# Kernel tuning notes

Measured on AMD Instinct MI355X. Metric: run time of the kernel, lower is better.

Reference implementation:

```python
import jax, jax.numpy as jnp
import numpy as np

MAX_SEQ_LEN = 2048
ADJ_SCALE = 0.1


def setup_inputs() -> dict:
    key = jax.random.key(0)
    k1, k2, k3 = jax.random.split(key, 3)
    B, L, H, D = 8, 2048, 16, 64
    x = jax.random.normal(k1, (B, L, H, D), dtype=jnp.float32)
    W = jax.random.normal(k2, (D, D), dtype=jnp.float32) * (1.0 / np.sqrt(D))
    b = jax.random.normal(k3, (D,), dtype=jnp.float32) * 0.02
    gate = jnp.ones((1,), dtype=jnp.float32) * 0.5  # betweenness_gate init
    return {"x": x, "W": W, "b": b, "gate": gate}


def reference(x, W, b, gate):
    B, L, H, D = x.shape
    # --- RoPE frequency table (precompute_freqs_cis) ---
    base_freqs = 1.0 / (10000.0 ** (jnp.arange(0, D, 2, dtype=jnp.float32) / D))  # (D/2,)
    t = jnp.arange(L, dtype=jnp.float32)
    freqs = t[:, None] * base_freqs[None, :]          # (L, D/2)
    fcos, fsin = jnp.cos(freqs), jnp.sin(freqs)

    # --- betweenness: only consecutive-pair distances are ever used ---
    content = jnp.einsum('blhd,ed->blhe', x, W) + b    # nn.Linear(dim, dim)
    d1 = jnp.linalg.norm(content[:, 1:] - content[:, :-1], axis=-1)   # (B, L-1, H)  d(i, i+1)
    d2 = jnp.linalg.norm(content[:, 2:] - content[:, :-2], axis=-1)   # (B, L-2, H)  d(i, i+2)
    direct = d2
    path = d1[:, :-1] + d1[:, 1:]
    score = jax.nn.relu(1.0 - (path - direct) / jnp.maximum(direct, 1e-6))  # (B, L-2, H)
    betweenness = jnp.zeros((B, L, H), x.dtype).at[:, 1:L - 1].set(score / (L - 2))

    # --- betweenness-adjusted interpolated RoPE (vectorized over positions) ---
    adjust = gate[0] * (betweenness - 0.5) * ADJ_SCALE               # (B, L, H)
    pos = jnp.arange(L, dtype=jnp.float32)[None, :, None]
    adj_pos = jnp.clip(pos + adjust, 0.0, MAX_SEQ_LEN - 1)
    lo = jnp.floor(adj_pos).astype(jnp.int32)
    hi = jnp.ceil(adj_pos).astype(jnp.int32)
    frac = (adj_pos - lo)[..., None]                                 # (B, L, H, 1)
    cos_i = (1.0 - frac) * fcos[lo] + frac * fcos[hi]                # (B, L, H, D/2)
    sin_i = (1.0 - frac) * fsin[lo] + frac * fsin[hi]

    x_even = x[..., 0::2]
    x_odd = x[..., 1::2]
    out_even = x_even * cos_i - x_odd * sin_i
    out_odd = x_odd * cos_i + x_even * sin_i
    out = jnp.stack([out_even, out_odd], axis=-1).reshape(B, L, H, D)  # re-interleave
    return out
```

## Files before the change

kernel.cpp:

```cpp
#include <hip/hip_runtime.h>

#define L_SEQ 2048
#define HEADS 16
#define DIM   64
#define TILE  32
#define XROWS 34
#define XPITCH 68
#define DROWS 48

typedef __attribute__((ext_vector_type(8))) short bf16x8;
typedef __attribute__((ext_vector_type(4))) float f32x4;

static __device__ __forceinline__ unsigned short f2bf_rtne(float f) {
    unsigned int u = __builtin_bit_cast(unsigned int, f);
    u += 0x7fffu + ((u >> 16) & 1u);
    return (unsigned short)(u >> 16);
}
static __device__ __forceinline__ unsigned int pk2(float a, float b) {
    return __builtin_amdgcn_perm(__builtin_bit_cast(unsigned int, b),
                                 __builtin_bit_cast(unsigned int, a), 0x07060302u);
}

#define SWZ(row, col) ((row) * 64 + ((col) ^ (((row) & 7) * 8)))

__global__ void prep_w_kernel(const float* __restrict__ W, unsigned short* __restrict__ wbf) {
    int i = blockIdx.x * 256 + threadIdx.x;
    if (i < DIM * DIM) wbf[i] = f2bf_rtne(W[i]);
}

static __device__ __forceinline__ bf16x8 load_bfrag(const unsigned short* wbf,
                                                    const float* W, int n, int k0) {
    if (wbf) return *(const bf16x8*)(wbf + n * 64 + k0);
    const float* wr = W + n * 64 + k0;
    float4 w0 = *(const float4*)wr;
    float4 w1 = *(const float4*)(wr + 4);
    uint4 p;
    p.x = pk2(w0.x, w0.y); p.y = pk2(w0.z, w0.w);
    p.z = pk2(w1.x, w1.y); p.w = pk2(w1.z, w1.w);
    return __builtin_bit_cast(bf16x8, p);
}

__global__ __launch_bounds__(256) void betweenness_rope_kernel(
    const float* __restrict__ x, const float* __restrict__ W,
    const unsigned short* __restrict__ wbf, const float* __restrict__ gate,
    float* __restrict__ out)
{
    __shared__ float xs[XROWS * XPITCH];
    __shared__ unsigned short dl[DROWS * 64];
    __shared__ float psq[4][36];
    __shared__ float ppr[4][36];
    __shared__ float2 fl[TILE];

    const int tid  = threadIdx.x;
    const int lane = tid & 63;
    const int wv   = tid >> 6;
    const int la   = lane & 15, lg = lane >> 4;
    const int l0   = blockIdx.x * TILE;
    const int h    = blockIdx.y;
    const int b    = blockIdx.z;
    const int bh_off = (b * L_SEQ * HEADS + h) * DIM;

    for (int c = tid; c < XROWS * 16; c += 256) {
        int r = c >> 4, q = c & 15;
        int g = max(0, min(L_SEQ - 1, l0 - 1 + r));
        *(float4*)&xs[r * XPITCH + q * 4] =
            *(const float4*)(x + bh_off + g * (HEADS * DIM) + q * 4);
    }
    __syncthreads();

    for (int r = tid >> 3; r < DROWS; r += 32) {
        int c0 = (tid & 7) * 8;
        uint4 o = {0u, 0u, 0u, 0u};
        if (r <= 32) {
            float4 a0 = *(float4*)&xs[r * XPITCH + c0];
            float4 a1 = *(float4*)&xs[r * XPITCH + c0 + 4];
            float4 b0 = *(float4*)&xs[(r + 1) * XPITCH + c0];
            float4 b1 = *(float4*)&xs[(r + 1) * XPITCH + c0 + 4];
            o.x = pk2(b0.x - a0.x, b0.y - a0.y);
            o.y = pk2(b0.z - a0.z, b0.w - a0.w);
            o.z = pk2(b1.x - a1.x, b1.y - a1.y);
            o.w = pk2(b1.z - a1.z, b1.w - a1.w);
        }
        *(uint4*)&dl[SWZ(r, c0)] = o;
    }
    __syncthreads();

    {
        bf16x8 b0 = load_bfrag(wbf, W, 16 * wv + la, lg * 8);
        bf16x8 b1 = load_bfrag(wbf, W, 16 * wv + la, lg * 8 + 32);
        f32x4 e0 = {0.f,0.f,0.f,0.f}, e1 = {0.f,0.f,0.f,0.f}, e2 = {0.f,0.f,0.f,0.f};
        {
            bf16x8 aA0 = *(const bf16x8*)&dl[SWZ(la,      lg * 8)];
            bf16x8 aA1 = *(const bf16x8*)&dl[SWZ(la,      lg * 8 + 32)];
            bf16x8 aB0 = *(const bf16x8*)&dl[SWZ(16 + la, lg * 8)];
            bf16x8 aB1 = *(const bf16x8*)&dl[SWZ(16 + la, lg * 8 + 32)];
            bf16x8 aC0 = *(const bf16x8*)&dl[SWZ(32 + la, lg * 8)];
            bf16x8 aC1 = *(const bf16x8*)&dl[SWZ(32 + la, lg * 8 + 32)];
            e0 = __builtin_amdgcn_mfma_f32_16x16x32_bf16(aA0, b0, e0, 0, 0, 0);
            e0 = __builtin_amdgcn_mfma_f32_16x16x32_bf16(aA1, b1, e0, 0, 0, 0);
            e1 = __builtin_amdgcn_mfma_f32_16x16x32_bf16(aB0, b0, e1, 0, 0, 0);
            e1 = __builtin_amdgcn_mfma_f32_16x16x32_bf16(aB1, b1, e1, 0, 0, 0);
            e2 = __builtin_amdgcn_mfma_f32_16x16x32_bf16(aC0, b0, e2, 0, 0, 0);
            e2 = __builtin_amdgcn_mfma_f32_16x16x32_bf16(aC1, b1, e2, 0, 0, 0);
        }
        float upA = __shfl(e0[0], (lane + 16) & 63);
        float upB = __shfl(e1[0], (lane + 16) & 63);
        float upC = __shfl(e2[0], (lane + 16) & 63);
        float sq0[4], sq1[4], pr0[4], pr1[4], sq2;
        #pragma unroll
        for (int q = 0; q < 4; ++q) { sq0[q] = e0[q] * e0[q]; sq1[q] = e1[q] * e1[q]; }
        sq2 = e2[0] * e2[0];
        #pragma unroll
        for (int q = 0; q < 3; ++q) { pr0[q] = e0[q] * e0[q + 1]; pr1[q] = e1[q] * e1[q + 1]; }
        pr0[3] = e0[3] * ((lg == 3) ? upB : upA);
        pr1[3] = e1[3] * ((lg == 3) ? upC : upB);
        #pragma unroll
        for (int m = 1; m < 16; m <<= 1) {
            #pragma unroll
            for (int q = 0; q < 4; ++q) {
                sq0[q] += __shfl_xor(sq0[q], m, 64);
                sq1[q] += __shfl_xor(sq1[q], m, 64);
                pr0[q] += __shfl_xor(pr0[q], m, 64);
                pr1[q] += __shfl_xor(pr1[q], m, 64);
            }
            sq2 += __shfl_xor(sq2, m, 64);
        }
        if (la == 0) {
            #pragma unroll
            for (int q = 0; q < 4; ++q) {
                psq[wv][4 * lg + q] = sq0[q];
                ppr[wv][4 * lg + q] = pr0[q];
            }
        } else if (la == 1) {
            #pragma unroll
            for (int q = 0; q < 4; ++q) {
                psq[wv][16 + 4 * lg + q] = sq1[q];
                ppr[wv][16 + 4 * lg + q] = pr1[q];
            }
        } else if (la == 2 && lg == 0) {
            psq[wv][32] = sq2;
        }
    }
    __syncthreads();

    if (tid < TILE) {
        const float gate0 = gate[0];
        int r = tid, l = l0 + r;
        float n1a = psq[0][r]     + psq[1][r]     + psq[2][r]     + psq[3][r];
        float n1b = psq[0][r + 1] + psq[1][r + 1] + psq[2][r + 1] + psq[3][r + 1];
        float gg  = ppr[0][r]     + ppr[1][r]     + ppr[2][r]     + ppr[3][r];
        float d1a = sqrtf(n1a), d1b = sqrtf(n1b);
        float dd  = sqrtf(fmaxf(n1a + n1b + 2.f * gg, 0.f));
        float sc  = fmaxf(1.f - ((d1a + d1b) - dd) / fmaxf(dd, 1e-6f), 0.f);
        float bet = (l >= 1 && l <= L_SEQ - 2) ? sc * (1.f / (L_SEQ - 2)) : 0.f;
        float adjust = gate0 * (bet - 0.5f) * 0.1f;
        float ap  = fminf(fmaxf((float)l + adjust, 0.f), (float)(L_SEQ - 1));
        float flo = floorf(ap);
        fl[r] = make_float2(flo, ap - flo);
    }
    __syncthreads();

    {
        const int j = lane & 31, half = lane >> 5;
        const float fjr = __builtin_exp2f(-0.4152410118609203f * (float)j)
                        * 0.15915494309189535f;
        const float cf = __builtin_amdgcn_cosf(fjr);
        const float sf = __builtin_amdgcn_sinf(fjr);
        const float cfm1 = cf - 1.0f;
        const int r0w = wv * 2 + half;
        const float* xbase = &xs[(r0w + 1) * XPITCH + 2 * j];
        float* obase = out + bh_off + (l0 + r0w) * (HEADS * DIM) + 2 * j;
        #pragma unroll
        for (int it = 0; it < 4; ++it) {
            int r = it * 8 + r0w;
            float2 ff = fl[r];
            float t0 = ff.x * fjr;
            float rv = t0 - floorf(t0);
            float c_lo = __builtin_amdgcn_cosf(rv);
            float s_lo = __builtin_amdgcn_sinf(rv);
            float u = fmaf(ff.y, cfm1, 1.0f);
            float v = ff.y * sf;
            float ci = fmaf(-s_lo, v, c_lo * u);
            float si = fmaf(c_lo, v, s_lo * u);
            float2 xv = *(const float2*)(xbase + it * 8 * XPITCH);
            float2 o;
            o.x = xv.x * ci - xv.y * si;
            o.y = fmaf(xv.y, ci, xv.x * si);
            *(float2*)(obase + it * 8 * (HEADS * DIM)) = o;
        }
    }
}

extern "C" void kernel_launch(void* const* d_in, const int* in_sizes, int n_in,
                              void* d_out, int out_size, void* d_ws, size_t ws_size,
                              hipStream_t stream) {
    const float* x    = (const float*)d_in[0];
    const float* W    = (const float*)d_in[1];
    const float* gate = (const float*)d_in[3];
    float* out = (float*)d_out;

    const int B = in_sizes[0] / (L_SEQ * HEADS * DIM);

    unsigned short* wbf = nullptr;
    if (ws_size >= (size_t)(DIM * DIM * sizeof(unsigned short))) {
        wbf = (unsigned short*)d_ws;
        prep_w_kernel<<<16, 256, 0, stream>>>(W, wbf);
    }

    dim3 grid(L_SEQ / TILE, HEADS, B);
    betweenness_rope_kernel<<<grid, 256, 0, stream>>>(x, W, wbf, gate, out);
}
```

Before: 50.15 us.

## Use Gram matrix W^T W for consecutive-diff norms and fuse diff into load

Precomputes M = W^T W in a small prep kernel and stores it in bf16 in a device global. The main kernel then computes each squared norm and adjacent inner product as d^T M d and d_{i+1}^T M d_i via MFMA plus a short dot product. This replaces the old per-row output reductions, which needed many cross-lane shuffles. The bf16 row differences are now built straight from global loads while filling the x tile, which removes one shared-memory pass and one barrier. In exchange, each x row is read twice from global memory, and bf16 rounding of M adds some error.

```diff
diff --git a/kernel.cpp b/kernel.cpp
--- a/kernel.cpp
+++ b/kernel.cpp
@@ -11,6 +11,8 @@
 typedef __attribute__((ext_vector_type(8))) short bf16x8;
 typedef __attribute__((ext_vector_type(4))) float f32x4;
 
+__device__ unsigned short g_mbf[DIM * DIM];
+
 static __device__ __forceinline__ unsigned short f2bf_rtne(float f) {
     unsigned int u = __builtin_bit_cast(unsigned int, f);
     u += 0x7fffu + ((u >> 16) & 1u);
@@ -20,35 +22,32 @@
     return __builtin_amdgcn_perm(__builtin_bit_cast(unsigned int, b),
                                  __builtin_bit_cast(unsigned int, a), 0x07060302u);
 }
+static __device__ __forceinline__ float bfhi(unsigned int u) {
+    return __builtin_bit_cast(float, u << 16);
+}
+static __device__ __forceinline__ float bflo(unsigned int u) {
+    return __builtin_bit_cast(float, u & 0xffff0000u);
+}
 
 #define SWZ(row, col) ((row) * 64 + ((col) ^ (((row) & 7) * 8)))
 
-__global__ void prep_w_kernel(const float* __restrict__ W, unsigned short* __restrict__ wbf) {
-    int i = blockIdx.x * 256 + threadIdx.x;
-    if (i < DIM * DIM) wbf[i] = f2bf_rtne(W[i]);
-}
-
-static __device__ __forceinline__ bf16x8 load_bfrag(const unsigned short* wbf,
-                                                    const float* W, int n, int k0) {
-    if (wbf) return *(const bf16x8*)(wbf + n * 64 + k0);
-    const float* wr = W + n * 64 + k0;
-    float4 w0 = *(const float4*)wr;
-    float4 w1 = *(const float4*)(wr + 4);
-    uint4 p;
-    p.x = pk2(w0.x, w0.y); p.y = pk2(w0.z, w0.w);
-    p.z = pk2(w1.x, w1.y); p.w = pk2(w1.z, w1.w);
-    return __builtin_bit_cast(bf16x8, p);
+__global__ void prep_m_kernel(const float* __restrict__ W) {
+    const int i = blockIdx.x, j = threadIdx.x;
+    float acc = 0.f;
+    #pragma unroll 8
+    for (int e = 0; e < DIM; ++e)
+        acc = fmaf(W[e * DIM + i], W[e * DIM + j], acc);
+    g_mbf[i * DIM + j] = f2bf_rtne(acc);
 }
 
 __global__ __launch_bounds__(256) void betweenness_rope_kernel(
-    const float* __restrict__ x, const float* __restrict__ W,
-    const unsigned short* __restrict__ wbf, const float* __restrict__ gate,
+    const float* __restrict__ x, const float* __restrict__ gate,
     float* __restrict__ out)
 {
     __shared__ float xs[XROWS * XPITCH];
     __shared__ unsigned short dl[DROWS * 64];
-    __shared__ float psq[4][36];
-    __shared__ float ppr[4][36];
+    __shared__ float psq[4][DROWS];
+    __shared__ float ppr[4][DROWS];
     __shared__ float2 fl[TILE];
 
     const int tid  = threadIdx.x;
@@ -60,85 +59,65 @@
     const int b    = blockIdx.z;
     const int bh_off = (b * L_SEQ * HEADS + h) * DIM;
 
-    for (int c = tid; c < XROWS * 16; c += 256) {
-        int r = c >> 4, q = c & 15;
-        int g = max(0, min(L_SEQ - 1, l0 - 1 + r));
-        *(float4*)&xs[r * XPITCH + q * 4] =
-            *(const float4*)(x + bh_off + g * (HEADS * DIM) + q * 4);
-    }
-    __syncthreads();
-
-    for (int r = tid >> 3; r < DROWS; r += 32) {
-        int c0 = (tid & 7) * 8;
-        uint4 o = {0u, 0u, 0u, 0u};
-        if (r <= 32) {
-            float4 a0 = *(float4*)&xs[r * XPITCH + c0];
-            float4 a1 = *(float4*)&xs[r * XPITCH + c0 + 4];
-            float4 b0 = *(float4*)&xs[(r + 1) * XPITCH + c0];
-            float4 b1 = *(float4*)&xs[(r + 1) * XPITCH + c0 + 4];
-            o.x = pk2(b0.x - a0.x, b0.y - a0.y);
-            o.y = pk2(b0.z - a0.z, b0.w - a0.w);
-            o.z = pk2(b1.x - a1.x, b1.y - a1.y);
-            o.w = pk2(b1.z - a1.z, b1.w - a1.w);
+    for (int s = tid; s < 392; s += 256) {
+        if (s < 272) {
+            int r = s >> 3, c0 = (s & 7) * 8;
+            int g = max(0, min(L_SEQ - 1, l0 - 1 + r));
+            const float* px = x + bh_off + g * (HEADS * DIM) + c0;
+            float4 x0 = *(const float4*)px;
+            float4 x1 = *(const float4*)(px + 4);
+            *(float4*)&xs[r * XPITCH + c0]     = x0;
+            *(float4*)&xs[r * XPITCH + c0 + 4] = x1;
+            if (r < 33) {
+                int g1 = min(L_SEQ - 1, l0 + r);
+                const float* py = x + bh_off + g1 * (HEADS * DIM) + c0;
+                float4 y0 = *(const float4*)py;
+                float4 y1 = *(const float4*)(py + 4);
+                uint4 o;
+                o.x = pk2(y0.x - x0.x, y0.y - x0.y);
+                o.y = pk2(y0.z - x0.z, y0.w - x0.w);
+                o.z = pk2(y1.x - x1.x, y1.y - x1.y);
+                o.w = pk2(y1.z - x1.z, y1.w - x1.w);
+                *(uint4*)&dl[SWZ(r, c0)] = o;
+            }
+        } else {
+            int z = s - 272;
+            int r = 33 + (z >> 3), c0 = (z & 7) * 8;
+            uint4 o = {0u, 0u, 0u, 0u};
+            *(uint4*)&dl[SWZ(r, c0)] = o;
         }
-        *(uint4*)&dl[SWZ(r, c0)] = o;
     }
     __syncthreads();
 
     {
-        bf16x8 b0 = load_bfrag(wbf, W, 16 * wv + la, lg * 8);
-        bf16x8 b1 = load_bfrag(wbf, W, 16 * wv + la, lg * 8 + 32);
-        f32x4 e0 = {0.f,0.f,0.f,0.f}, e1 = {0.f,0.f,0.f,0.f}, e2 = {0.f,0.f,0.f,0.f};
-        {
-            bf16x8 aA0 = *(const bf16x8*)&dl[SWZ(la,      lg * 8)];
-            bf16x8 aA1 = *(const bf16x8*)&dl[SWZ(la,      lg * 8 + 32)];
-            bf16x8 aB0 = *(const bf16x8*)&dl[SWZ(16 + la, lg * 8)];
-            bf16x8 aB1 = *(const bf16x8*)&dl[SWZ(16 + la, lg * 8 + 32)];
-            bf16x8 aC0 = *(const bf16x8*)&dl[SWZ(32 + la, lg * 8)];
-            bf16x8 aC1 = *(const bf16x8*)&dl[SWZ(32 + la, lg * 8 + 32)];
-            e0 = __builtin_amdgcn_mfma_f32_16x16x32_bf16(aA0, b0, e0, 0, 0, 0);
-            e0 = __builtin_amdgcn_mfma_f32_16x16x32_bf16(aA1, b1, e0, 0, 0, 0);
-            e1 = __builtin_amdgcn_mfma_f32_16x16x32_bf16(aB0, b0, e1, 0, 0, 0);
-            e1 = __builtin_amdgcn_mfma_f32_16x16x32_bf16(aB1, b1, e1, 0, 0, 0);
-            e2 = __builtin_amdgcn_mfma_f32_16x16x32_bf16(aC0, b0, e2, 0, 0, 0);
-            e2 = __builtin_amdgcn_mfma_f32_16x16x32_bf16(aC1, b1, e2, 0, 0, 0);
-        }
-        float upA = __shfl(e0[0], (lane + 16) & 63);
-        float upB = __shfl(e1[0], (lane + 16) & 63);
-        float upC = __shfl(e2[0], (lane + 16) & 63);
-        float sq0[4], sq1[4], pr0[4], pr1[4], sq2;
+        const int abase = (16 * wv + la) * 64 + lg * 8;
+        bf16x8 ma0 = *(const bf16x8*)&g_mbf[abase];
+        bf16x8 ma1 = *(const bf16x8*)&g_mbf[abase + 32];
+        const int c = 16 * wv + 4 * lg;
         #pragma unroll
-        for (int q = 0; q < 4; ++q) { sq0[q] = e0[q] * e0[q]; sq1[q] = e1[q] * e1[q]; }
-        sq2 = e2[0] * e2[0];
-        #pragma unroll
-        for (int q = 0; q < 3; ++q) { pr0[q] = e0[q] * e0[q + 1]; pr1[q] = e1[q] * e1[q + 1]; }
-        pr0[3] = e0[3] * ((lg == 3) ? upB : upA);
-        pr1[3] = e1[3] * ((lg == 3) ? upC : upB);
-        #pragma unroll
-        for (int m = 1; m < 16; m <<= 1) {
-            #pragma unroll
-            for (int q = 0; q < 4; ++q) {
-                sq0[q] += __shfl_xor(sq0[q], m, 64);
-                sq1[q] += __shfl_xor(sq1[q], m, 64);
-                pr0[q] += __shfl_xor(pr0[q], m, 64);
-                pr1[q] += __shfl_xor(pr1[q], m, 64);
-            }
-            sq2 += __shfl_xor(sq2, m, 64);
-        }
-        if (la == 0) {
-            #pragma unroll
-            for (int q = 0; q < 4; ++q) {
-                psq[wv][4 * lg + q] = sq0[q];
-                ppr[wv][4 * lg + q] = pr0[q];
-            }
-        } else if (la == 1) {
-            #pragma unroll
-            for (int q = 0; q < 4; ++q) {
-                psq[wv][16 + 4 * lg + q] = sq1[q];
-                ppr[wv][16 + 4 * lg + q] = pr1[q];
-            }
-        } else if (la == 2 && lg == 0) {
-            psq[wv][32] = sq2;
+        for (int rt = 0; rt < 3; ++rt) {
+            int br = 16 * rt + la;
+            bf16x8 bb0 = *(const bf16x8*)&dl[SWZ(br, lg * 8)];
+            bf16x8 bb1 = *(const bf16x8*)&dl[SWZ(br, lg * 8 + 32)];
+            f32x4 d = {0.f, 0.f, 0.f, 0.f};
+            d = __builtin_amdgcn_mfma_f32_16x16x32_bf16(ma0, bb0, d, 0, 0, 0);
+            d = __builtin_amdgcn_mfma_f32_16x16x32_bf16(ma1, bb1, d, 0, 0, 0);
+            uint2 duv = *(const uint2*)&dl[SWZ(br, c)];
+            int br1 = min(br + 1, DROWS - 1);
+            uint2 dvv = *(const uint2*)&dl[SWZ(br1, c)];
+            float n1p = d[0] * bfhi(duv.x);
+            n1p = fmaf(d[1], bflo(duv.x), n1p);
+            n1p = fmaf(d[2], bfhi(duv.y), n1p);
+            n1p = fmaf(d[3], bflo(duv.y), n1p);
+            float g1p = d[0] * bfhi(dvv.x);
+            g1p = fmaf(d[1], bflo(dvv.x), g1p);
+            g1p = fmaf(d[2], bfhi(dvv.y), g1p);
+            g1p = fmaf(d[3], bflo(dvv.y), g1p);
+            n1p += __shfl_xor(n1p, 16, 64);
+            g1p += __shfl_xor(g1p, 16, 64);
+            n1p += __shfl_xor(n1p, 32, 64);
+            g1p += __shfl_xor(g1p, 32, 64);
+            if (lg == 0) { psq[wv][br] = n1p; ppr[wv][br] = g1p; }
         }
     }
     __syncthreads();
@@ -201,12 +180,8 @@
 
     const int B = in_sizes[0] / (L_SEQ * HEADS * DIM);
 
-    unsigned short* wbf = nullptr;
-    if (ws_size >= (size_t)(DIM * DIM * sizeof(unsigned short))) {
-        wbf = (unsigned short*)d_ws;
-        prep_w_kernel<<<16, 256, 0, stream>>>(W, wbf);
-    }
+    prep_m_kernel<<<DIM, DIM, 0, stream>>>(W);
 
     dim3 grid(L_SEQ / TILE, HEADS, B);
-    betweenness_rope_kernel<<<grid, 256, 0, stream>>>(x, W, wbf, gate, out);
+    betweenness_rope_kernel<<<grid, 256, 0, stream>>>(x, gate, out);
 }
```

Result: faster. 42.76 us (-14.7%).
